# Kernel tuning notes

Hardware: AMD Instinct MI355X
Metric: run time of the kernel (lower is better)

## Reference

```python
import jax, jax.numpy as jnp
import numpy as np

B, N, C, K = 8, 4096, 512, 150

def setup_inputs() -> dict:
    key = jax.random.key(0)
    ks = jax.random.split(key, 10)
    std_c = float(np.sqrt(2.0 / C))
    x = jax.random.normal(ks[0], (B, N, C), dtype=jnp.float32)
    Wq = jax.random.normal(ks[1], (K, C), dtype=jnp.float32) * std_c
    bq = jnp.zeros((K,), dtype=jnp.float32)
    Wk = jax.random.normal(ks[2], (K, C), dtype=jnp.float32) * std_c
    bk = jnp.zeros((K,), dtype=jnp.float32)
    Wv = jax.random.normal(ks[3], (C, C), dtype=jnp.float32) * std_c
    bv = jnp.zeros((C,), dtype=jnp.float32)
    # original inits mlp_res to zeros; use small random so output is nontrivial
    Wres = jax.random.normal(ks[4], (C, C), dtype=jnp.float32) * (0.02)
    bres = jnp.zeros((C,), dtype=jnp.float32)
    gamma = jnp.full((1,), 0.5, dtype=jnp.float32)  # original init is 0; nonzero for testing
    return {"x": x, "Wq": Wq, "bq": bq, "Wk": Wk, "bk": bk,
            "Wv": Wv, "bv": bv, "Wres": Wres, "bres": bres, "gamma": gamma}

def reference(x, Wq, bq, Wk, bk, Wv, bv, Wres, bres, gamma):
    # seg_map: (B,N,K); seg_ft: (B,N,K); feats: (B,N,C)
    seg_map = jnp.einsum('bnc,kc->bnk', x, Wq) + bq
    seg_ft = jnp.einsum('bnc,kc->bnk', x, Wk) + bk
    v = jnp.einsum('bnc,dc->bnd', x, Wv) + bv
    # low-rank QK^T -> (B,N,N), unscaled, row softmax
    score = jnp.einsum('bnk,bmk->bnm', seg_map, seg_ft)
    score = jax.nn.softmax(score, axis=-1)
    feats = jnp.einsum('bnm,bmd->bnd', score, v)
    feats = jnp.einsum('bnd,ed->bne', feats, Wres) + bres
    # dropout omitted (inference); gamma-gated residual
    feat_map = gamma * feats + x
    return (seg_map, feat_map)
```

## Files before the change

kernel.cpp:

```cpp
#include <hip/hip_runtime.h>
#include <cstdint>
#include <cstddef>

#define M_ROWS 32768
#define CDIM   512
#define KRANK  150
#define KPAD   160

typedef __bf16 bf16x8 __attribute__((ext_vector_type(8)));
typedef float  f32x4  __attribute__((ext_vector_type(4)));

union U16B { uint4 u; bf16x8 b; };
static __device__ __forceinline__ bf16x8 u2b(uint4 u) { U16B x; x.u = u; return x.b; }

static __device__ __forceinline__ unsigned short f2bf(float f) {
  uint32_t u = __float_as_uint(f);
  u += 0x7fffu + ((u >> 16) & 1u);
  return (unsigned short)(u >> 16);
}

static __device__ __forceinline__ void cvt8(float4 a, float4 b, uint4& h, uint4& l) {
  float v[8] = {a.x, a.y, a.z, a.w, b.x, b.y, b.z, b.w};
  unsigned short hs[8], ls[8];
#pragma unroll
  for (int i = 0; i < 8; ++i) {
    hs[i] = f2bf(v[i]);
    const float hf = __uint_as_float((uint32_t)hs[i] << 16);
    ls[i] = f2bf(v[i] - hf);
  }
  h = *(uint4*)&hs[0];
  l = *(uint4*)&ls[0];
}

static __device__ __forceinline__ void glds16(const void* g, void* l) {
  __builtin_amdgcn_global_load_lds(
      (const __attribute__((address_space(1))) unsigned int*)g,
      (__attribute__((address_space(3))) unsigned int*)l, 16, 0, 0);
}

static __device__ __forceinline__ int sa16f(int row, int k4) {
  return ((row >> 1) << 3) + ((((row & 1) << 2) | k4) ^ ((row >> 1) & 7));
}

__global__ __launch_bounds__(512)
void cvt_all(const float* __restrict__ X, unsigned short* __restrict__ Ximg,
             const float* __restrict__ Wv, const float* __restrict__ Wres,
             const float* __restrict__ Wq, const float* __restrict__ Wk,
             unsigned short* __restrict__ WvC, unsigned short* __restrict__ WresC,
             unsigned short* __restrict__ WqC, unsigned short* __restrict__ WkC)
{
  const int tid = threadIdx.x;
  const int srow = tid >> 2, sk4 = tid & 3;
  const int sa = sa16f(srow, sk4);

  if (blockIdx.x < 4096) {
    const int bid = blockIdx.x;
    const int mt = bid >> 4, kt = bid & 15;
    const float* xp = X + (size_t)(mt * 128 + srow) * 512 + kt * 32 + sk4 * 8;
    const float4 v0 = *(const float4*)(xp);
    const float4 v1 = *(const float4*)(xp + 4);
    uint4 h4, l4; cvt8(v0, v1, h4, l4);
    unsigned short* ib = Ximg + (size_t)bid * 8192;
    *(uint4*)&ib[(size_t)sa * 8]         = h4;
    *(uint4*)&ib[(size_t)(512 + sa) * 8] = l4;
    return;
  }

  int job = blockIdx.x - 4096;
  const float* W; unsigned short* img; int N;
  if (job < 32)      { W = Wv;   img = WvC;   N = 512; }
  else if (job < 64) { W = Wres; img = WresC; N = 512; job -= 32; }
  else if (job < 80) { W = Wq;   img = WqC;   N = KRANK; job -= 64; }
  else               { W = Wk;   img = WkC;   N = KRANK; job -= 80; }
  const int nt = (N == 512) ? (job >> 4) : 0;
  const int kt = job & 15;

  unsigned short* ib = img + (size_t)(nt * 16 + kt) * 16384;
#pragma unroll
  for (int h = 0; h < 2; ++h) {
    const int row = nt * 256 + h * 128 + srow;
    float4 v0 = make_float4(0.f, 0.f, 0.f, 0.f), v1 = v0;
    if (row < N) {
      v0 = *(const float4*)&W[(size_t)row * 512 + kt * 32 + sk4 * 8];
      v1 = *(const float4*)&W[(size_t)row * 512 + kt * 32 + sk4 * 8 + 4];
    }
    uint4 h4, l4; cvt8(v0, v1, h4, l4);
    const int cell = h * 512 + sa;
    *(uint4*)&ib[(size_t)cell * 8]          = h4;
    *(uint4*)&ib[(size_t)(1024 + cell) * 8] = l4;
  }
}

template<int MODE, int AGL>
__global__ __launch_bounds__(512, 4)
void mgemm_nt(const float* __restrict__ A, const unsigned short* __restrict__ Ximg,
              const unsigned short* __restrict__ Wimg,
              const float* __restrict__ bias, float* __restrict__ out,
              const float* __restrict__ xres, const float* __restrict__ gammap,
              unsigned short* __restrict__ aux,
              const unsigned short* __restrict__ Wimg2,
              const float* __restrict__ bias2,
              unsigned short* __restrict__ aux2)
{
  __shared__ __align__(16) unsigned short lds[24576];
  constexpr int NI  = (MODE == 5) ? 2 : 4;
  constexpr int NJ  = (MODE == 5) ? 5 : 4;
  constexpr int NCW = (MODE == 5) ? 80 : 64;
  const int tid = threadIdx.x;
  const int m0  = blockIdx.y * 128;
  const int bx  = blockIdx.x;

  const unsigned short* img = (MODE == 5) ? (bx ? Wimg2 : Wimg)
                                          : Wimg + (size_t)(bx * 16) * 16384;
  const float* bias_u = (MODE == 5 && bx) ? bias2 : bias;
  unsigned short* aux_u = (MODE == 5 && bx) ? aux2 : aux;

  const int srow = tid >> 2, sk4 = tid & 3;
  const int sa16 = sa16f(srow, sk4);
  const float* ap = A + (size_t)(m0 + srow) * 512 + sk4 * 8;

  const int lane = tid & 63, w = tid >> 6;
  const int wm = (MODE == 5) ? (w >> 1) : (w >> 2);
  const int wn = (MODE == 5) ? (w & 1) : (w & 3);
  const int arb = wm * ((MODE == 5) ? 32 : 64);
  const int cq = lane & 15, quad = lane >> 4;
  const int fsub = (((cq & 1) << 2) | quad) ^ (cq >> 1);
  const int foff = ((cq >> 1) << 3) + fsub;

  const unsigned short* ibase = img + (size_t)(w * 64 + lane) * 8;
  const unsigned short* xibase = Ximg + (size_t)(m0 >> 7) * 16 * 8192
                               + (size_t)(w * 64 + lane) * 8;

  f32x4 acc[NI][NJ];
#pragma unroll
  for (int i = 0; i < NI; ++i)
#pragma unroll
    for (int j = 0; j < NJ; ++j) acc[i][j] = (f32x4){0.f, 0.f, 0.f, 0.f};

  for (int kt = 0; kt < 512; kt += 32) {
    uint4 ahi, alo;
    if (AGL == 0) {
      const float4 av0 = *(const float4*)(ap + kt);
      const float4 av1 = *(const float4*)(ap + kt + 4);
      cvt8(av0, av1, ahi, alo);
    }

    __syncthreads();
    if (AGL == 0) {
      *(uint4*)&lds[       sa16 * 8] = ahi;
      *(uint4*)&lds[4096 + sa16 * 8] = alo;
    } else {
      const unsigned short* xs = xibase + (size_t)(kt >> 5) * 8192;
      glds16(xs,                   &lds[(w * 64) * 8]);
      glds16(xs + (size_t)512 * 8, &lds[4096 + (w * 64) * 8]);
    }
    const unsigned short* src = ibase + (size_t)(kt >> 5) * 16384;
    if (MODE == 5) {
      glds16(src,                         &lds[8192 + (w * 64) * 8]);
      if (w < 2) glds16(src + 4096,       &lds[8192 + (512 + w * 64) * 8]);
      glds16(src + 8192,                  &lds[8192 + (1024 + w * 64) * 8]);
      if (w < 2) glds16(src + 12288,      &lds[8192 + (1536 + w * 64) * 8]);
    } else {
#pragma unroll
      for (int c = 0; c < 4; ++c)
        glds16(src + (size_t)c * 4096, &lds[8192 + (c * 512 + w * 64) * 8]);
    }
    __syncthreads();

    bf16x8 ah[NI], al_[NI];
#pragma unroll
    for (int i = 0; i < NI; ++i) {
      const int ac = (arb + i * 16) * 4 + foff;
      ah[i]  = u2b(*(const uint4*)&lds[       ac * 8]);
      al_[i] = u2b(*(const uint4*)&lds[4096 + ac * 8]);
    }
#pragma unroll
    for (int j = 0; j < NJ; ++j) {
      const int rb = wn * NCW + j * 16;
      const int bc = (rb >> 7) * 512 + (rb & 127) * 4 + foff;
      const bf16x8 bh = u2b(*(const uint4*)&lds[8192  + bc * 8]);
      const bf16x8 bl = u2b(*(const uint4*)&lds[16384 + bc * 8]);
#pragma unroll
      for (int i = 0; i < NI; ++i) {
        acc[i][j] = __builtin_amdgcn_mfma_f32_16x16x32_bf16(ah[i],  bh, acc[i][j], 0, 0, 0);
        acc[i][j] = __builtin_amdgcn_mfma_f32_16x16x32_bf16(al_[i], bh, acc[i][j], 0, 0, 0);
        acc[i][j] = __builtin_amdgcn_mfma_f32_16x16x32_bf16(ah[i],  bl, acc[i][j], 0, 0, 0);
      }
    }
  }

  const int n0b = (MODE == 5) ? 0 : bx * 256;
  const int mb = m0 + arb + quad * 4;
  const int nb = n0b + wn * NCW + cq;

  if (MODE == 1) {
    const float g = gammap[0];
#pragma unroll
    for (int j = 0; j < NJ; ++j) {
      const float bvj = bias_u[nb + j * 16];
#pragma unroll
      for (int i = 0; i < NI; ++i) {
#pragma unroll
        for (int r = 0; r < 4; ++r) {
          const size_t off = (size_t)(mb + i * 16 + r) * 512 + (nb + j * 16);
          out[off] = fmaf(g, acc[i][j][r] + bvj, xres[off]);
        }
      }
    }
  } else if (MODE == 4) {
    const int b = m0 >> 12;
    const int key0 = (m0 & 4095) + arb + quad * 4;
#pragma unroll
    for (int j = 0; j < NJ; ++j) {
      const float bvj = bias_u[nb + j * 16];
      const size_t rowo = (size_t)(b * 512 + nb + j * 16) * 4096;
#pragma unroll
      for (int i = 0; i < NI; ++i) {
        unsigned short o4[4];
#pragma unroll
        for (int r = 0; r < 4; ++r) o4[r] = f2bf(acc[i][j][r] + bvj);
        uint2 o;
        o.x = (unsigned int)o4[0] | ((unsigned int)o4[1] << 16);
        o.y = (unsigned int)o4[2] | ((unsigned int)o4[3] << 16);
        *(uint2*)&aux_u[rowo + key0 + i * 16] = o;
      }
    }
  } else {
#pragma unroll
    for (int j = 0; j < NJ; ++j) {
      const int n = nb + j * 16;
      const float bvj = (n < KRANK) ? bias_u[n] : 0.f;
#pragma unroll
      for (int i = 0; i < NI; ++i) {
#pragma unroll
        for (int r = 0; r < 4; ++r) {
          const int m = mb + i * 16 + r;
          float v = (n < KRANK) ? (acc[i][j][r] + bvj) : 0.f;
          if (bx == 0 && n < KRANK) out[(size_t)m * KRANK + n] = v;
          const unsigned short hh = f2bf(v);
          aux_u[(size_t)m * 320 + n] = hh;
          const float hf = __uint_as_float(((uint32_t)hh) << 16);
          aux_u[(size_t)m * 320 + 160 + n] = f2bf(v - hf);
        }
      }
    }
  }
}

__global__ __launch_bounds__(512, 2)
void attn_mfma(const unsigned short* __restrict__ Qc,
               const unsigned short* __restrict__ Kc,
               const unsigned short* __restrict__ VT,
               float* __restrict__ O)
{
  __shared__ __align__(16) unsigned short smem[32592];
  unsigned short* klds = smem;
  unsigned short* vtl  = smem + 10496;
  unsigned short* plds = smem + 26944;
  float*    alw   = (float*)(smem + 32064);
  unsigned* updf  = (unsigned*)(smem + 32320);
  float*    linvp = (float*)(smem + 32336);

  const int bid = blockIdx.x;
  const int b   = bid & 7;
  const int qt  = bid >> 3;
  const int r0  = (b << 12) + qt * 128;

  const int tid  = threadIdx.x;
  const int w    = tid >> 6;
  const int lane = tid & 63;
  const int quad = lane >> 4;
  const int cq   = lane & 15;
  const int p    = w >> 1;
  const int h    = w & 1;

  bf16x8 qhi[5], qlo[5];
  {
    const size_t qrow = (size_t)(r0 + w * 16 + cq) * 320;
#pragma unroll
    for (int c = 0; c < 5; ++c) {
      qhi[c] = u2b(*(const uint4*)(Qc + qrow + c * 32 + quad * 8));
      qlo[c] = u2b(*(const uint4*)(Qc + qrow + 160 + c * 32 + quad * 8));
    }
  }

  f32x4 acc4[32];
#pragma unroll
  for (int i = 0; i < 32; ++i) acc4[i] = (f32x4){0.f, 0.f, 0.f, 0.f};
  float mreg = -3.0e38f, lreg = 0.f;

  const int vqd = (tid & 3) * 8;
  const int vc  = tid >> 2;
  const int vwb = (tid & 3) * 4112 + vc * 8;
  const int vrb = quad * 4112 + h * 2048 + cq * 8;

  const int krow0 = tid / 40,          kc0 = (tid - krow0 * 40) * 8;
  const int krow1 = (tid + 512) / 40,  kc1 = ((tid + 512) - krow1 * 40) * 8;
  const int krow2 = (tid + 1024) / 40, kc2 = ((tid + 1024) - krow2 * 40) * 8;

  uint4 pk0, pk1, pk2, pv0, pv1, pv2, pv3;
  const unsigned short* kbase = Kc + (size_t)(b * 4096) * 320;
  const unsigned short* vbase = VT + ((size_t)(b * 512 + vc)) * 4096 + vqd;
  {
    pk0 = *(const uint4*)(kbase + (size_t)tid * 8);
    pk1 = *(const uint4*)(kbase + (size_t)(tid + 512) * 8);
    if (tid < 256) pk2 = *(const uint4*)(kbase + (size_t)(tid + 1024) * 8);
    pv0 = *(const uint4*)(vbase);
    pv1 = *(const uint4*)(vbase + (size_t)128 * 4096);
    pv2 = *(const uint4*)(vbase + (size_t)256 * 4096);
    pv3 = *(const uint4*)(vbase + (size_t)384 * 4096);
  }

  for (int kt = 0; kt < 128; ++kt) {
    __syncthreads();

    *(uint4*)&klds[krow0 * 328 + kc0] = pk0;
    *(uint4*)&klds[krow1 * 328 + kc1] = pk1;
    if (tid < 256) *(uint4*)&klds[krow2 * 328 + kc2] = pk2;
    *(uint4*)&vtl[vwb]        = pv0;
    *(uint4*)&vtl[vwb + 1024] = pv1;
    *(uint4*)&vtl[vwb + 2048] = pv2;
    *(uint4*)&vtl[vwb + 3072] = pv3;

    __syncthreads();

    {
      const int ktn = (kt < 127) ? kt + 1 : 127;
      pk0 = *(const uint4*)(kbase + (size_t)(ktn * 32 * 320) + (size_t)tid * 8);
      pk1 = *(const uint4*)(kbase + (size_t)(ktn * 32 * 320) + (size_t)(tid + 512) * 8);
      if (tid < 256) pk2 = *(const uint4*)(kbase + (size_t)(ktn * 32 * 320) + (size_t)(tid + 1024) * 8);
      pv0 = *(const uint4*)(vbase + ktn * 32);
      pv1 = *(const uint4*)(vbase + (size_t)128 * 4096 + ktn * 32);
      pv2 = *(const uint4*)(vbase + (size_t)256 * 4096 + ktn * 32);
      pv3 = *(const uint4*)(vbase + (size_t)384 * 4096 + ktn * 32);
    }

    f32x4 S0 = (f32x4){0.f, 0.f, 0.f, 0.f};
    f32x4 S1 = (f32x4){0.f, 0.f, 0.f, 0.f};
    __builtin_amdgcn_s_setprio(1);
#pragma unroll
    for (int c = 0; c < 5; ++c) {
      const int ko = c * 32 + quad * 8;
      const bf16x8 kh0 = u2b(*(const uint4*)&klds[cq * 328 + ko]);
      const bf16x8 kl0 = u2b(*(const uint4*)&klds[cq * 328 + 160 + ko]);
      const bf16x8 kh1 = u2b(*(const uint4*)&klds[(16 + cq) * 328 + ko]);
      const bf16x8 kl1 = u2b(*(const uint4*)&klds[(16 + cq) * 328 + 160 + ko]);
      S0 = __builtin_amdgcn_mfma_f32_16x16x32_bf16(kh0, qhi[c], S0, 0, 0, 0);
      S1 = __builtin_amdgcn_mfma_f32_16x16x32_bf16(kh1, qhi[c], S1, 0, 0, 0);
      S0 = __builtin_amdgcn_mfma_f32_16x16x32_bf16(kl0, qhi[c], S0, 0, 0, 0);
      S1 = __builtin_amdgcn_mfma_f32_16x16x32_bf16(kl1, qhi[c], S1, 0, 0, 0);
      S0 = __builtin_amdgcn_mfma_f32_16x16x32_bf16(kh0, qlo[c], S0, 0, 0, 0);
      S1 = __builtin_amdgcn_mfma_f32_16x16x32_bf16(kh1, qlo[c], S1, 0, 0, 0);
    }
    __builtin_amdgcn_s_setprio(0);

    unsigned short* pw = plds + w * 640;
    float t = fmaxf(fmaxf(S0[0], S0[1]), fmaxf(S0[2], S0[3]));
    t = fmaxf(t, fmaxf(fmaxf(S1[0], S1[1]), fmaxf(S1[2], S1[3])));
    t = fmaxf(t, __shfl_xor(t, 16));
    t = fmaxf(t, __shfl_xor(t, 32));
    const bool need = (t > mreg + 8.f);
    const float mn = need ? t : mreg;
    const float al = need ? __expf(mreg - mn) : 1.f;
    mreg = mn;
    float pv[8];
#pragma unroll
    for (int r = 0; r < 4; ++r) { pv[r] = __expf(S0[r] - mn); pv[4 + r] = __expf(S1[r] - mn); }
    float ts = ((pv[0] + pv[1]) + (pv[2] + pv[3])) + ((pv[4] + pv[5]) + (pv[6] + pv[7]));
    ts += __shfl_xor(ts, 16);
    ts += __shfl_xor(ts, 32);
    lreg = lreg * al + ts;
    {
      unsigned short q0 = f2bf(pv[0]), q1 = f2bf(pv[1]), q2 = f2bf(pv[2]), q3 = f2bf(pv[3]);
      unsigned short q4 = f2bf(pv[4]), q5 = f2bf(pv[5]), q6 = f2bf(pv[6]), q7 = f2bf(pv[7]);
      uint2 o0, o1;
      o0.x = (unsigned)q0 | ((unsigned)q1 << 16); o0.y = (unsigned)q2 | ((unsigned)q3 << 16);
      o1.x = (unsigned)q4 | ((unsigned)q5 << 16); o1.y = (unsigned)q6 | ((unsigned)q7 << 16);
      *(uint2*)&pw[cq * 40 + quad * 4]      = o0;
      *(uint2*)&pw[cq * 40 + 16 + quad * 4] = o1;
    }
    if (lane < 16) alw[w * 16 + lane] = al;
    const bool anyu = __any(need);
    if (lane == 0) updf[w] = anyu ? 1u : 0u;

    __syncthreads();

    const unsigned short* pb = plds + (2 * p) * 640 + cq * 40 + quad * 8;
    const bf16x8 pa0 = u2b(*(const uint4*)pb);
    const bf16x8 pa1 = u2b(*(const uint4*)(pb + 640));

    if (updf[2 * p] | updf[2 * p + 1]) {
      float aA[4], aB[4];
#pragma unroll
      for (int r = 0; r < 4; ++r) {
        aA[r] = alw[(2 * p) * 16 + quad * 4 + r];
        aB[r] = alw[(2 * p + 1) * 16 + quad * 4 + r];
      }
#pragma unroll
      for (int ct = 0; ct < 16; ++ct) {
#pragma unroll
        for (int r = 0; r < 4; ++r) {
          acc4[ct][r]      *= aA[r];
          acc4[16 + ct][r] *= aB[r];
        }
      }
    }

    __builtin_amdgcn_s_setprio(1);
#pragma unroll
    for (int ct = 0; ct < 16; ++ct) {
      const bf16x8 vb = u2b(*(const uint4*)&vtl[vrb + ct * 128]);
      acc4[ct]      = __builtin_amdgcn_mfma_f32_16x16x32_bf16(pa0, vb, acc4[ct], 0, 0, 0);
      acc4[16 + ct] = __builtin_amdgcn_mfma_f32_16x16x32_bf16(pa1, vb, acc4[16 + ct], 0, 0, 0);
    }
    __builtin_amdgcn_s_setprio(0);
  }

  if (lane < 16) linvp[w * 16 + lane] = 1.f / lreg;
  __syncthreads();

  float invv[2][4];
#pragma unroll
  for (int rt = 0; rt < 2; ++rt)
#pragma unroll
    for (int r = 0; r < 4; ++r)
      invv[rt][r] = linvp[(2 * p + rt) * 16 + quad * 4 + r];

  float* ep = (float*)smem + w * 1088;
#pragma unroll
  for (int rt = 0; rt < 2; ++rt) {
    const int rowb = r0 + (2 * p + rt) * 16;
#pragma unroll
    for (int g = 0; g < 4; ++g) {
#pragma unroll
      for (int ii = 0; ii < 4; ++ii)
#pragma unroll
        for (int r = 0; r < 4; ++r)
          ep[(quad * 4 + r) * 68 + ii * 16 + cq] = acc4[rt * 16 + g * 4 + ii][r] * invv[rt][r];
#pragma unroll
      for (int t = 0; t < 4; ++t) {
        const int flat4 = t * 64 + lane;
        const int row = flat4 >> 4;
        const int c4 = flat4 & 15;
        const float4 val = *(const float4*)&ep[row * 68 + c4 * 4];
        *(float4*)&O[(size_t)(rowb + row) * CDIM + h * 256 + g * 64 + c4 * 4] = val;
      }
    }
  }
}

extern "C" void kernel_launch(void* const* d_in, const int* in_sizes, int n_in,
                              void* d_out, int out_size, void* d_ws, size_t ws_size,
                              hipStream_t stream)
{
  const float* x     = (const float*)d_in[0];
  const float* Wq    = (const float*)d_in[1];
  const float* bq    = (const float*)d_in[2];
  const float* Wk    = (const float*)d_in[3];
  const float* bk    = (const float*)d_in[4];
  const float* Wv    = (const float*)d_in[5];
  const float* bv    = (const float*)d_in[6];
  const float* Wres  = (const float*)d_in[7];
  const float* bres  = (const float*)d_in[8];
  const float* gamma = (const float*)d_in[9];

  float* seg_map  = (float*)d_out;
  float* feat_map = seg_map + (size_t)M_ROWS * KRANK;

  unsigned short* Qcomb = (unsigned short*)d_ws;
  unsigned short* Kcomb = Qcomb + (size_t)M_ROWS * 320;
  unsigned short* VTb   = Kcomb + (size_t)M_ROWS * 320;
  float*          feats = (float*)(VTb + (size_t)M_ROWS * CDIM);
  unsigned short* WvC   = (unsigned short*)(feats + (size_t)M_ROWS * CDIM);
  unsigned short* WresC = WvC   + (size_t)2 * 16 * 16384;
  unsigned short* WqC   = WresC + (size_t)2 * 16 * 16384;
  unsigned short* WkC   = WqC   + (size_t)16 * 16384;
  unsigned short* XiC   = (unsigned short*)feats;

  cvt_all<<<dim3(4192), dim3(512), 0, stream>>>(x, XiC, Wv, Wres, Wq, Wk, WvC, WresC, WqC, WkC);
  mgemm_nt<5, 1><<<dim3(2, 256), dim3(512), 0, stream>>>(x, XiC, WqC, bq, seg_map, nullptr, nullptr, Qcomb, WkC, bk, Kcomb);
  mgemm_nt<4, 1><<<dim3(2, 256), dim3(512), 0, stream>>>(x, XiC, WvC, bv, nullptr, nullptr, nullptr, VTb, nullptr, nullptr, nullptr);
  attn_mfma<<<dim3(256), dim3(512), 0, stream>>>(Qcomb, Kcomb, VTb, feats);
  mgemm_nt<1, 0><<<dim3(2, 256), dim3(512), 0, stream>>>(feats, nullptr, WresC, bres, feat_map, x, gamma, nullptr, nullptr, nullptr, nullptr);
}
```

Before: 671.8 us.

## Double-buffer K/V tiles with direct global-to-LDS loads and XOR swizzle

Replaces register-staged K and V prefetch with direct global-to-LDS copies (glds16) into double-buffered shared memory. The next tile's loads are issued after the softmax barrier so they overlap the PV MFMAs. K and V LDS layouts gain an XOR swizzle to avoid bank conflicts on the 16-byte reads. The probability tile and the alpha/update flags are also double-buffered, which leaves one barrier per iteration on that path. The cost is that shared memory roughly doubles to about 128KB per block, which likely drops occupancy below the two blocks per CU declared in launch bounds.

Result: no change. 679.0 us (+1.1%).

```diff
diff --git a/kernel.cpp b/kernel.cpp
--- a/kernel.cpp
+++ b/kernel.cpp
@@ -253,13 +253,8 @@
                const unsigned short* __restrict__ VT,
                float* __restrict__ O)
 {
-  __shared__ __align__(16) unsigned short smem[32592];
-  unsigned short* klds = smem;
-  unsigned short* vtl  = smem + 10496;
-  unsigned short* plds = smem + 26944;
-  float*    alw   = (float*)(smem + 32064);
-  unsigned* updf  = (unsigned*)(smem + 32320);
-  float*    linvp = (float*)(smem + 32336);
+  __shared__ __align__(16) unsigned short smem[64288];
+  constexpr int KB = 0, VB = 20480, PB = 53248, AW = 63488, UF = 64000, LV = 64032;
 
   const int bid = blockIdx.x;
   const int b   = bid & 7;
@@ -271,6 +266,7 @@
   const int lane = tid & 63;
   const int quad = lane >> 4;
   const int cq   = lane & 15;
+  const int cqx  = cq & 7;
   const int p    = w >> 1;
   const int h    = w & 1;
 
@@ -289,62 +285,59 @@
   for (int i = 0; i < 32; ++i) acc4[i] = (f32x4){0.f, 0.f, 0.f, 0.f};
   float mreg = -3.0e38f, lreg = 0.f;
 
-  const int vqd = (tid & 3) * 8;
-  const int vc  = tid >> 2;
-  const int vwb = (tid & 3) * 4112 + vc * 8;
-  const int vrb = quad * 4112 + h * 2048 + cq * 8;
-
-  const int krow0 = tid / 40,          kc0 = (tid - krow0 * 40) * 8;
-  const int krow1 = (tid + 512) / 40,  kc1 = ((tid + 512) - krow1 * 40) * 8;
-  const int krow2 = (tid + 1024) / 40, kc2 = ((tid + 1024) - krow2 * 40) * 8;
-
-  uint4 pk0, pk1, pk2, pv0, pv1, pv2, pv3;
   const unsigned short* kbase = Kc + (size_t)(b * 4096) * 320;
-  const unsigned short* vbase = VT + ((size_t)(b * 512 + vc)) * 4096 + vqd;
+  int koff0, koff1, koff2;
   {
-    pk0 = *(const uint4*)(kbase + (size_t)tid * 8);
-    pk1 = *(const uint4*)(kbase + (size_t)(tid + 512) * 8);
-    if (tid < 256) pk2 = *(const uint4*)(kbase + (size_t)(tid + 1024) * 8);
-    pv0 = *(const uint4*)(vbase);
-    pv1 = *(const uint4*)(vbase + (size_t)128 * 4096);
-    pv2 = *(const uint4*)(vbase + (size_t)256 * 4096);
-    pv3 = *(const uint4*)(vbase + (size_t)384 * 4096);
-  }
+    int cell, key, c4l, oc4;
+    cell = w * 64 + lane;        key = cell / 40; c4l = cell - key * 40;
+    oc4 = (c4l & 56) | ((c4l & 7) ^ (key & 7)); koff0 = key * 320 + oc4 * 8;
+    cell = (8 + w) * 64 + lane;  key = cell / 40; c4l = cell - key * 40;
+    oc4 = (c4l & 56) | ((c4l & 7) ^ (key & 7)); koff1 = key * 320 + oc4 * 8;
+    cell = (16 + w) * 64 + lane; key = cell / 40; c4l = cell - key * 40;
+    oc4 = (c4l & 56) | ((c4l & 7) ^ (key & 7)); koff2 = key * 320 + oc4 * 8;
+  }
+  const unsigned short *vp0, *vp1, *vp2, *vp3;
+  {
+    int Lp, g, L;
+    Lp = (w * 4 + 0) * 64 + lane; g = Lp >> 3; L = (g << 3) | ((Lp & 7) ^ (g & 7));
+    vp0 = VT + ((size_t)(b * 512 + (L >> 2))) * 4096 + (L & 3) * 8;
+    Lp = (w * 4 + 1) * 64 + lane; g = Lp >> 3; L = (g << 3) | ((Lp & 7) ^ (g & 7));
+    vp1 = VT + ((size_t)(b * 512 + (L >> 2))) * 4096 + (L & 3) * 8;
+    Lp = (w * 4 + 2) * 64 + lane; g = Lp >> 3; L = (g << 3) | ((Lp & 7) ^ (g & 7));
+    vp2 = VT + ((size_t)(b * 512 + (L >> 2))) * 4096 + (L & 3) * 8;
+    Lp = (w * 4 + 3) * 64 + lane; g = Lp >> 3; L = (g << 3) | ((Lp & 7) ^ (g & 7));
+    vp3 = VT + ((size_t)(b * 512 + (L >> 2))) * 4096 + (L & 3) * 8;
+  }
+  const int vlo = h * 8192 + ((cq >> 1) << 6) + ((((cq & 1) * 4 + quad) ^ (cq >> 1)) << 3);
+
+  {
+    unsigned short* kd = &smem[KB];
+    glds16(kbase + koff0, kd + w * 512);
+    glds16(kbase + koff1, kd + (8 + w) * 512);
+    if (w < 4) glds16(kbase + koff2, kd + (16 + w) * 512);
+    unsigned short* vd = &smem[VB + (w * 4) * 512];
+    glds16(vp0, vd);        glds16(vp1, vd + 512);
+    glds16(vp2, vd + 1024); glds16(vp3, vd + 1536);
+  }
+  __syncthreads();
 
   for (int kt = 0; kt < 128; ++kt) {
-    __syncthreads();
-
-    *(uint4*)&klds[krow0 * 328 + kc0] = pk0;
-    *(uint4*)&klds[krow1 * 328 + kc1] = pk1;
-    if (tid < 256) *(uint4*)&klds[krow2 * 328 + kc2] = pk2;
-    *(uint4*)&vtl[vwb]        = pv0;
-    *(uint4*)&vtl[vwb + 1024] = pv1;
-    *(uint4*)&vtl[vwb + 2048] = pv2;
-    *(uint4*)&vtl[vwb + 3072] = pv3;
-
-    __syncthreads();
-
-    {
-      const int ktn = (kt < 127) ? kt + 1 : 127;
-      pk0 = *(const uint4*)(kbase + (size_t)(ktn * 32 * 320) + (size_t)tid * 8);
-      pk1 = *(const uint4*)(kbase + (size_t)(ktn * 32 * 320) + (size_t)(tid + 512) * 8);
-      if (tid < 256) pk2 = *(const uint4*)(kbase + (size_t)(ktn * 32 * 320) + (size_t)(tid + 1024) * 8);
-      pv0 = *(const uint4*)(vbase + ktn * 32);
-      pv1 = *(const uint4*)(vbase + (size_t)128 * 4096 + ktn * 32);
-      pv2 = *(const uint4*)(vbase + (size_t)256 * 4096 + ktn * 32);
-      pv3 = *(const uint4*)(vbase + (size_t)384 * 4096 + ktn * 32);
-    }
+    const int buf = kt & 1;
+    const unsigned short* k0 = &smem[KB + buf * 10240] + cq * 320;
+    const unsigned short* k1 = k0 + 16 * 320;
 
     f32x4 S0 = (f32x4){0.f, 0.f, 0.f, 0.f};
     f32x4 S1 = (f32x4){0.f, 0.f, 0.f, 0.f};
     __builtin_amdgcn_s_setprio(1);
 #pragma unroll
     for (int c = 0; c < 5; ++c) {
-      const int ko = c * 32 + quad * 8;
-      const bf16x8 kh0 = u2b(*(const uint4*)&klds[cq * 328 + ko]);
-      const bf16x8 kl0 = u2b(*(const uint4*)&klds[cq * 328 + 160 + ko]);
-      const bf16x8 kh1 = u2b(*(const uint4*)&klds[(16 + cq) * 328 + ko]);
-      const bf16x8 kl1 = u2b(*(const uint4*)&klds[(16 + cq) * 328 + 160 + ko]);
+      const int thi = c * 4 + quad, tlo = thi + 20;
+      const int ohi = ((thi & 56) | ((thi & 7) ^ cqx)) * 8;
+      const int olo = ((tlo & 56) | ((tlo & 7) ^ cqx)) * 8;
+      const bf16x8 kh0 = u2b(*(const uint4*)(k0 + ohi));
+      const bf16x8 kl0 = u2b(*(const uint4*)(k0 + olo));
+      const bf16x8 kh1 = u2b(*(const uint4*)(k1 + ohi));
+      const bf16x8 kl1 = u2b(*(const uint4*)(k1 + olo));
       S0 = __builtin_amdgcn_mfma_f32_16x16x32_bf16(kh0, qhi[c], S0, 0, 0, 0);
       S1 = __builtin_amdgcn_mfma_f32_16x16x32_bf16(kh1, qhi[c], S1, 0, 0, 0);
       S0 = __builtin_amdgcn_mfma_f32_16x16x32_bf16(kl0, qhi[c], S0, 0, 0, 0);
@@ -354,7 +347,7 @@
     }
     __builtin_amdgcn_s_setprio(0);
 
-    unsigned short* pw = plds + w * 640;
+    unsigned short* pw = &smem[PB + buf * 5120 + w * 640];
     float t = fmaxf(fmaxf(S0[0], S0[1]), fmaxf(S0[2], S0[3]));
     t = fmaxf(t, fmaxf(fmaxf(S1[0], S1[1]), fmaxf(S1[2], S1[3])));
     t = fmaxf(t, __shfl_xor(t, 16));
@@ -363,38 +356,53 @@
     const float mn = need ? t : mreg;
     const float al = need ? __expf(mreg - mn) : 1.f;
     mreg = mn;
-    float pv[8];
-#pragma unroll
-    for (int r = 0; r < 4; ++r) { pv[r] = __expf(S0[r] - mn); pv[4 + r] = __expf(S1[r] - mn); }
-    float ts = ((pv[0] + pv[1]) + (pv[2] + pv[3])) + ((pv[4] + pv[5]) + (pv[6] + pv[7]));
+    float pvx[8];
+#pragma unroll
+    for (int r = 0; r < 4; ++r) { pvx[r] = __expf(S0[r] - mn); pvx[4 + r] = __expf(S1[r] - mn); }
+    float ts = ((pvx[0] + pvx[1]) + (pvx[2] + pvx[3])) + ((pvx[4] + pvx[5]) + (pvx[6] + pvx[7]));
     ts += __shfl_xor(ts, 16);
     ts += __shfl_xor(ts, 32);
     lreg = lreg * al + ts;
     {
-      unsigned short q0 = f2bf(pv[0]), q1 = f2bf(pv[1]), q2 = f2bf(pv[2]), q3 = f2bf(pv[3]);
-      unsigned short q4 = f2bf(pv[4]), q5 = f2bf(pv[5]), q6 = f2bf(pv[6]), q7 = f2bf(pv[7]);
+      unsigned short q0 = f2bf(pvx[0]), q1 = f2bf(pvx[1]), q2 = f2bf(pvx[2]), q3 = f2bf(pvx[3]);
+      unsigned short q4 = f2bf(pvx[4]), q5 = f2bf(pvx[5]), q6 = f2bf(pvx[6]), q7 = f2bf(pvx[7]);
       uint2 o0, o1;
       o0.x = (unsigned)q0 | ((unsigned)q1 << 16); o0.y = (unsigned)q2 | ((unsigned)q3 << 16);
       o1.x = (unsigned)q4 | ((unsigned)q5 << 16); o1.y = (unsigned)q6 | ((unsigned)q7 << 16);
       *(uint2*)&pw[cq * 40 + quad * 4]      = o0;
       *(uint2*)&pw[cq * 40 + 16 + quad * 4] = o1;
     }
-    if (lane < 16) alw[w * 16 + lane] = al;
+    float* alwB = (float*)&smem[AW] + buf * 128;
+    if (lane < 16) alwB[w * 16 + lane] = al;
+    unsigned* updB = (unsigned*)&smem[UF] + buf * 8;
     const bool anyu = __any(need);
-    if (lane == 0) updf[w] = anyu ? 1u : 0u;
+    if (lane == 0) updB[w] = anyu ? 1u : 0u;
 
     __syncthreads();
 
-    const unsigned short* pb = plds + (2 * p) * 640 + cq * 40 + quad * 8;
+    if (kt < 127) {
+      const int nbuf = buf ^ 1;
+      const unsigned short* ks = kbase + (size_t)(kt + 1) * 10240;
+      unsigned short* kd = &smem[KB + nbuf * 10240];
+      glds16(ks + koff0, kd + w * 512);
+      glds16(ks + koff1, kd + (8 + w) * 512);
+      if (w < 4) glds16(ks + koff2, kd + (16 + w) * 512);
+      const int vo = (kt + 1) * 32;
+      unsigned short* vd = &smem[VB + nbuf * 16384 + (w * 4) * 512];
+      glds16(vp0 + vo, vd);        glds16(vp1 + vo, vd + 512);
+      glds16(vp2 + vo, vd + 1024); glds16(vp3 + vo, vd + 1536);
+    }
+
+    const unsigned short* pb = &smem[PB + buf * 5120 + (2 * p) * 640 + cq * 40 + quad * 8];
     const bf16x8 pa0 = u2b(*(const uint4*)pb);
     const bf16x8 pa1 = u2b(*(const uint4*)(pb + 640));
 
-    if (updf[2 * p] | updf[2 * p + 1]) {
+    if (updB[2 * p] | updB[2 * p + 1]) {
       float aA[4], aB[4];
 #pragma unroll
       for (int r = 0; r < 4; ++r) {
-        aA[r] = alw[(2 * p) * 16 + quad * 4 + r];
-        aB[r] = alw[(2 * p + 1) * 16 + quad * 4 + r];
+        aA[r] = alwB[(2 * p) * 16 + quad * 4 + r];
+        aB[r] = alwB[(2 * p + 1) * 16 + quad * 4 + r];
       }
 #pragma unroll
       for (int ct = 0; ct < 16; ++ct) {
@@ -406,16 +414,20 @@
       }
     }
 
+    const unsigned short* vbL = &smem[VB + buf * 16384] + vlo;
     __builtin_amdgcn_s_setprio(1);
 #pragma unroll
     for (int ct = 0; ct < 16; ++ct) {
-      const bf16x8 vb = u2b(*(const uint4*)&vtl[vrb + ct * 128]);
+      const bf16x8 vb = u2b(*(const uint4*)(vbL + ct * 512));
       acc4[ct]      = __builtin_amdgcn_mfma_f32_16x16x32_bf16(pa0, vb, acc4[ct], 0, 0, 0);
       acc4[16 + ct] = __builtin_amdgcn_mfma_f32_16x16x32_bf16(pa1, vb, acc4[16 + ct], 0, 0, 0);
     }
     __builtin_amdgcn_s_setprio(0);
-  }
-
+
+    __syncthreads();
+  }
+
+  float* linvp = (float*)&smem[LV];
   if (lane < 16) linvp[w * 16 + lane] = 1.f / lreg;
   __syncthreads();
 
@@ -438,8 +450,8 @@
         for (int r = 0; r < 4; ++r)
           ep[(quad * 4 + r) * 68 + ii * 16 + cq] = acc4[rt * 16 + g * 4 + ii][r] * invv[rt][r];
 #pragma unroll
-      for (int t = 0; t < 4; ++t) {
-        const int flat4 = t * 64 + lane;
+      for (int t2 = 0; t2 < 4; ++t2) {
+        const int flat4 = t2 * 64 + lane;
         const int row = flat4 >> 4;
         const int c4 = flat4 & 15;
         const float4 val = *(const float4*)&ep[row * 68 + c4 * 4];
```
